# Optimization experiments

Measured on AMD Instinct MI355X. Metric: run time of the kernel, lower is better.

## Reference

```python
import jax, jax.numpy as jnp
import numpy as np

B, N, D2H, U = 16, 1024, 1024, 512  # batch of sentences, tokens, 2*lstm_dims, hidden_units


def setup_inputs() -> dict:
    key = jax.random.key(0)
    ks = jax.random.split(key, 7)
    s = 1.0 / np.sqrt(D2H)
    return {
        "x": jax.random.normal(ks[0], (B, N, D2H), dtype=jnp.float32),
        "W_h": jax.random.normal(ks[1], (U, D2H), dtype=jnp.float32) * s,
        "b_h": jax.random.normal(ks[2], (U,), dtype=jnp.float32) * 0.01,
        "W_m": jax.random.normal(ks[3], (U, D2H), dtype=jnp.float32) * s,
        "b_m": jax.random.normal(ks[4], (U,), dtype=jnp.float32) * 0.01,
        "w_out": jax.random.normal(ks[5], (U,), dtype=jnp.float32) * (1.0 / np.sqrt(U)),
        "b_out": jax.random.normal(ks[6], (), dtype=jnp.float32) * 0.01,
    }


def reference(x, W_h, b_h, W_m, b_m, w_out, b_out):
    # headfov[i] = W_h @ x_i + b_h ; modfov[j] = W_m @ x_j + b_m
    H = jnp.einsum("bnd,ud->bnu", x, W_h) + b_h  # [B, N, U]
    M = jnp.einsum("bnd,ud->bnu", x, W_m) + b_m  # [B, N, U]
    # score[i,j] = w_out . (H_i + M_j) + b_out  (outLayer is linear, so it
    # distributes over the add; avoids materializing an [B,N,N,U] tensor)
    sH = jnp.einsum("bnu,u->bn", H, w_out)  # [B, N]
    sM = jnp.einsum("bnu,u->bn", M, w_out)  # [B, N]
    scores = sH[:, :, None] + sM[:, None, :] + b_out  # [B, N, N]
    return scores
```

## Files before the change

### kernel.cpp

```cpp
#include <hip/hip_runtime.h>

#define BB 16
#define NN 1024
#define DD 1024
#define UU 512

__global__ __launch_bounds__(256) void prep_kernel(
    const float* __restrict__ W_h, const float* __restrict__ W_m,
    const float* __restrict__ b_h, const float* __restrict__ b_m,
    const float* __restrict__ w_out, const float* __restrict__ b_out,
    float* __restrict__ v_h, float* __restrict__ v_m, float* __restrict__ Cc) {
    __shared__ float w_s[UU];
    int t = threadIdx.x;
    for (int u = t; u < UU; u += 256) w_s[u] = w_out[u];
    __syncthreads();

    if (blockIdx.x < 4) {
        int d = blockIdx.x * 256 + t;
        float ah = 0.f, am = 0.f;
        #pragma unroll 8
        for (int u = 0; u < UU; ++u) {
            float w = w_s[u];
            ah += W_h[(size_t)u * DD + d] * w;
            am += W_m[(size_t)u * DD + d] * w;
        }
        v_h[d] = ah;
        v_m[d] = am;
    } else {
        __shared__ float red[256];
        float acc = 0.f;
        for (int u = t; u < UU; u += 256) acc += (b_h[u] + b_m[u]) * w_s[u];
        red[t] = acc;
        __syncthreads();
        for (int s = 128; s > 0; s >>= 1) {
            if (t < s) red[t] += red[t + s];
            __syncthreads();
        }
        if (t == 0) *Cc = red[0] + b_out[0];
    }
}

__global__ __launch_bounds__(256) void row_dots_kernel(
    const float* __restrict__ x,
    const float* __restrict__ v_h, const float* __restrict__ v_m,
    float* __restrict__ sH, float* __restrict__ sM) {
    __shared__ float4 vh_s[DD / 4];
    __shared__ float4 vm_s[DD / 4];
    int t = threadIdx.x;
    vh_s[t] = ((const float4*)v_h)[t];
    vm_s[t] = ((const float4*)v_m)[t];
    __syncthreads();

    int wave = t >> 6;
    int lane = t & 63;
    int row = blockIdx.x * 4 + wave;
    const float4* xr = (const float4*)(x + (size_t)row * DD);

    float ah = 0.f, am = 0.f;
    #pragma unroll
    for (int k = 0; k < 4; ++k) {
        int idx = lane + 64 * k;
        float4 xv = xr[idx];
        float4 hv = vh_s[idx];
        float4 mv = vm_s[idx];
        ah += xv.x * hv.x + xv.y * hv.y + xv.z * hv.z + xv.w * hv.w;
        am += xv.x * mv.x + xv.y * mv.y + xv.z * mv.z + xv.w * mv.w;
    }
    #pragma unroll
    for (int off = 32; off > 0; off >>= 1) {
        ah += __shfl_down(ah, off, 64);
        am += __shfl_down(am, off, 64);
    }
    if (lane == 0) {
        sH[row] = ah;
        sM[row] = am;
    }
}

__global__ __launch_bounds__(256) void scores_kernel(
    const float* __restrict__ sH, const float* __restrict__ sM,
    const float* __restrict__ Cc, float4* __restrict__ out) {
    float C = *Cc;
    size_t t = (size_t)blockIdx.x * 256 + threadIdx.x;
    size_t idx = t << 2;
    int bi = (int)(idx >> 10);
    int j  = (int)(idx & 1023);
    float h = sH[bi] + C;
    float4 m = *(const float4*)(sM + (bi & ~1023) + j);
    float4 o;
    o.x = h + m.x;
    o.y = h + m.y;
    o.z = h + m.z;
    o.w = h + m.w;
    out[t] = o;
}

extern "C" void kernel_launch(void* const* d_in, const int* in_sizes, int n_in,
                              void* d_out, int out_size, void* d_ws, size_t ws_size,
                              hipStream_t stream) {
    const float* x     = (const float*)d_in[0];
    const float* W_h   = (const float*)d_in[1];
    const float* b_h   = (const float*)d_in[2];
    const float* W_m   = (const float*)d_in[3];
    const float* b_m   = (const float*)d_in[4];
    const float* w_out = (const float*)d_in[5];
    const float* b_out = (const float*)d_in[6];
    float* out = (float*)d_out;

    float* ws  = (float*)d_ws;
    float* sH  = ws;
    float* sM  = ws + 16384;
    float* v_h = ws + 32768;
    float* v_m = ws + 33792;
    float* Cc  = ws + 34816;

    prep_kernel<<<5, 256, 0, stream>>>(W_h, W_m, b_h, b_m, w_out, b_out, v_h, v_m, Cc);
    row_dots_kernel<<<BB * NN / 4, 256, 0, stream>>>(x, v_h, v_m, sH, sM);
    scores_kernel<<<(size_t)BB * NN * NN / 1024, 256, 0, stream>>>(sH, sM, Cc, (float4*)out);
}
```

Measured before the change: 150.1 us.

## Split W·w_out reduction across many blocks with atomics and simplify score indexing

The prep kernel now spreads the W_h/W_m matvec over 128 blocks, each summing a 32-row slice of U and combining results with atomicAdd into buffers zeroed by a memset, in place of 4 blocks each looping over all 512 rows. The row-dot kernel reads v_h/v_m directly from global memory without shared staging and folds the constant bias into sH. The scores kernel maps one block per output row, which removes the per-element bias load and the index arithmetic. This adds a memset launch and atomics, and float atomic ordering makes the sums nondeterministic.

```diff
diff --git a/kernel.cpp b/kernel.cpp
--- a/kernel.cpp
+++ b/kernel.cpp
@@ -10,26 +10,24 @@
     const float* __restrict__ b_h, const float* __restrict__ b_m,
     const float* __restrict__ w_out, const float* __restrict__ b_out,
     float* __restrict__ v_h, float* __restrict__ v_m, float* __restrict__ Cc) {
-    __shared__ float w_s[UU];
     int t = threadIdx.x;
-    for (int u = t; u < UU; u += 256) w_s[u] = w_out[u];
-    __syncthreads();
-
-    if (blockIdx.x < 4) {
-        int d = blockIdx.x * 256 + t;
-        float ah = 0.f, am = 0.f;
-        #pragma unroll 8
-        for (int u = 0; u < UU; ++u) {
-            float w = w_s[u];
-            ah += W_h[(size_t)u * DD + d] * w;
-            am += W_m[(size_t)u * DD + d] * w;
+    int blk = blockIdx.x;
+    if (blk < 128) {
+        const float* W = (blk < 64) ? W_h : W_m;
+        float* v = (blk < 64) ? v_h : v_m;
+        int b = blk & 63;
+        int d = (b & 3) * 256 + t;
+        int u0 = (b >> 2) * 32;
+        float acc = 0.f;
+        #pragma unroll
+        for (int k = 0; k < 32; ++k) {
+            acc += W[(size_t)(u0 + k) * DD + d] * w_out[u0 + k];
         }
-        v_h[d] = ah;
-        v_m[d] = am;
+        atomicAdd(v + d, acc);
     } else {
         __shared__ float red[256];
         float acc = 0.f;
-        for (int u = t; u < UU; u += 256) acc += (b_h[u] + b_m[u]) * w_s[u];
+        for (int u = t; u < UU; u += 256) acc += (b_h[u] + b_m[u]) * w_out[u];
         red[t] = acc;
         __syncthreads();
         for (int s = 128; s > 0; s >>= 1) {
@@ -43,26 +41,22 @@
 __global__ __launch_bounds__(256) void row_dots_kernel(
     const float* __restrict__ x,
     const float* __restrict__ v_h, const float* __restrict__ v_m,
+    const float* __restrict__ Cc,
     float* __restrict__ sH, float* __restrict__ sM) {
-    __shared__ float4 vh_s[DD / 4];
-    __shared__ float4 vm_s[DD / 4];
     int t = threadIdx.x;
-    vh_s[t] = ((const float4*)v_h)[t];
-    vm_s[t] = ((const float4*)v_m)[t];
-    __syncthreads();
-
-    int wave = t >> 6;
-    int lane = t & 63;
+    int wave = t >> 6, lane = t & 63;
     int row = blockIdx.x * 4 + wave;
     const float4* xr = (const float4*)(x + (size_t)row * DD);
+    const float4* vh = (const float4*)v_h;
+    const float4* vm = (const float4*)v_m;
 
     float ah = 0.f, am = 0.f;
     #pragma unroll
     for (int k = 0; k < 4; ++k) {
         int idx = lane + 64 * k;
         float4 xv = xr[idx];
-        float4 hv = vh_s[idx];
-        float4 mv = vm_s[idx];
+        float4 hv = vh[idx];
+        float4 mv = vm[idx];
         ah += xv.x * hv.x + xv.y * hv.y + xv.z * hv.z + xv.w * hv.w;
         am += xv.x * mv.x + xv.y * mv.y + xv.z * mv.z + xv.w * mv.w;
     }
@@ -72,27 +66,25 @@
         am += __shfl_down(am, off, 64);
     }
     if (lane == 0) {
-        sH[row] = ah;
+        sH[row] = ah + *Cc;
         sM[row] = am;
     }
 }
 
 __global__ __launch_bounds__(256) void scores_kernel(
     const float* __restrict__ sH, const float* __restrict__ sM,
-    const float* __restrict__ Cc, float4* __restrict__ out) {
-    float C = *Cc;
-    size_t t = (size_t)blockIdx.x * 256 + threadIdx.x;
-    size_t idx = t << 2;
-    int bi = (int)(idx >> 10);
-    int j  = (int)(idx & 1023);
-    float h = sH[bi] + C;
-    float4 m = *(const float4*)(sM + (bi & ~1023) + j);
+    float4* __restrict__ out) {
+    int bi = blockIdx.x;
+    int j4 = threadIdx.x;
+    float h = sH[bi];
+    const float4* mrow = (const float4*)(sM + (bi & ~(NN - 1)));
+    float4 m = mrow[j4];
     float4 o;
     o.x = h + m.x;
     o.y = h + m.y;
     o.z = h + m.z;
     o.w = h + m.w;
-    out[t] = o;
+    out[(size_t)bi * (NN / 4) + j4] = o;
 }
 
 extern "C" void kernel_launch(void* const* d_in, const int* in_sizes, int n_in,
@@ -108,13 +100,15 @@
     float* out = (float*)d_out;
 
     float* ws  = (float*)d_ws;
-    float* sH  = ws;
-    float* sM  = ws + 16384;
-    float* v_h = ws + 32768;
-    float* v_m = ws + 33792;
-    float* Cc  = ws + 34816;
+    float* v_h = ws;
+    float* v_m = ws + 1024;
+    float* Cc  = ws + 2048;
+    float* sH  = ws + 4096;
+    float* sM  = ws + 4096 + 16384;
 
-    prep_kernel<<<5, 256, 0, stream>>>(W_h, W_m, b_h, b_m, w_out, b_out, v_h, v_m, Cc);
-    row_dots_kernel<<<BB * NN / 4, 256, 0, stream>>>(x, v_h, v_m, sH, sM);
-    scores_kernel<<<(size_t)BB * NN * NN / 1024, 256, 0, stream>>>(sH, sM, Cc, (float4*)out);
+    hipMemsetAsync(ws, 0, 2048 * sizeof(float), stream);
+
+    prep_kernel<<<129, 256, 0, stream>>>(W_h, W_m, b_h, b_m, w_out, b_out, v_h, v_m, Cc);
+    row_dots_kernel<<<BB * NN / 4, 256, 0, stream>>>(x, v_h, v_m, Cc, sH, sM);
+    scores_kernel<<<BB * NN, 256, 0, stream>>>(sH, sM, (float4*)out);
 }
```

Result: faster. 127.6 us (-15.0%).
